# Optimization experiments

Hardware: AMD Instinct MI355X
Metric: run time of the kernel (lower is better)

The kernel has to match this reference:

```python
import jax, jax.numpy as jnp
import numpy as np
from jax import lax

DIM = 128
DEPTH = 2
OUT_DIM = 256
DIM_HEAD = 64
HEADS = 8
WS = 16
INNER = DIM_HEAD * HEADS
EPS = 1e-5
SCALE = DIM_HEAD ** (-0.5)


def setup_inputs() -> dict:
    key = jax.random.key(0)
    ks = jax.random.split(key, 20)
    s = 0.02
    L = DEPTH
    inp = {
        "x": jax.random.normal(ks[0], (1, DIM, 256, 256), dtype=jnp.float32),
        "ln1_g": jnp.ones((L, DIM), dtype=jnp.float32),
        "ln1_b": jnp.zeros((L, DIM), dtype=jnp.float32),
        "wq": jax.random.normal(ks[1], (L, INNER, DIM), dtype=jnp.float32) * s,
        "wkv": jax.random.normal(ks[2], (L, 2 * INNER, DIM), dtype=jnp.float32) * s,
        "wo": jax.random.normal(ks[3], (L, DIM, INNER), dtype=jnp.float32) * s,
        "bo": jnp.zeros((L, DIM), dtype=jnp.float32),
        "ln2_g": jnp.ones((L, DIM), dtype=jnp.float32),
        "ln2_b": jnp.zeros((L, DIM), dtype=jnp.float32),
        "w_in": jax.random.normal(ks[4], (L, DIM, DIM), dtype=jnp.float32) * s,
        "b_in": jnp.zeros((L, DIM), dtype=jnp.float32),
        "w_c3": jax.random.normal(ks[5], (L, OUT_DIM, DIM, 3, 3), dtype=jnp.float32) * s,
        "b_c3": jnp.zeros((L, OUT_DIM), dtype=jnp.float32),
        "w_c1": jax.random.normal(ks[6], (L, DIM, OUT_DIM), dtype=jnp.float32) * s,
        "b_c1": jnp.zeros((L, DIM), dtype=jnp.float32),
        "w_outer": jax.random.normal(ks[7], (DIM, DIM), dtype=jnp.float32) * s,
        "b_outer": jnp.zeros((DIM,), dtype=jnp.float32),
    }
    return inp


def _layernorm(x, g, b):
    # channel-wise (dim=1) norm; note torch code uses (std + eps), not sqrt(var + eps)
    mean = jnp.mean(x, axis=1, keepdims=True)
    std = jnp.sqrt(jnp.var(x, axis=1, keepdims=True))
    return (x - mean) / (std + EPS) * g[None, :, None, None] + b[None, :, None, None]


def _conv1x1(w, x, b=None):
    y = jnp.einsum('oi,bihw->bohw', w, x)
    if b is not None:
        y = y + b[None, :, None, None]
    return y


def _to_windows(t, B, H, W):
    # [B, HEADS*DIM_HEAD, H, W] -> [B*HEADS*nx*ny, WS*WS, DIM_HEAD]
    nx, ny = H // WS, W // WS
    t = t.reshape(B, HEADS, DIM_HEAD, nx, WS, ny, WS)
    t = t.transpose(0, 1, 3, 5, 4, 6, 2)
    return t.reshape(B * HEADS * nx * ny, WS * WS, DIM_HEAD)


def _from_windows(t, B, H, W):
    nx, ny = H // WS, W // WS
    t = t.reshape(B, HEADS, nx, ny, WS, WS, DIM_HEAD)
    t = t.transpose(0, 1, 6, 2, 4, 3, 5)
    return t.reshape(B, HEADS * DIM_HEAD, H, W)


def _attention(x, wq_l, wkv_l, wo_l, bo_l):
    B, _, H, W = x.shape
    q = _conv1x1(wq_l, x)
    kv = _conv1x1(wkv_l, x)
    k, v = kv[:, :INNER], kv[:, INNER:]
    q = _to_windows(q, B, H, W)
    k = _to_windows(k, B, H, W)
    v = _to_windows(v, B, H, W)
    sim = jnp.einsum('bid,bjd->bij', q, k) * SCALE  # [nwin, 256, 256]
    attn = jax.nn.softmax(sim, axis=-1)
    out = jnp.einsum('bij,bjd->bid', attn, v)
    out = _from_windows(out, B, H, W)
    return _conv1x1(wo_l, out, bo_l)


def _feedforward(x, w_in_l, b_in_l, w_c3_l, b_c3_l, w_c1_l, b_c1_l):
    h = _conv1x1(w_in_l, x, b_in_l)
    h = lax.conv_general_dilated(h, w_c3_l, window_strides=(1, 1), padding='SAME',
                                 dimension_numbers=('NCHW', 'OIHW', 'NCHW'))
    h = h + b_c3_l[None, :, None, None]
    h = jax.nn.gelu(h, approximate=False)
    return _conv1x1(w_c1_l, h, b_c1_l)


def reference(x, ln1_g, ln1_b, wq, wkv, wo, bo, ln2_g, ln2_b,
              w_in, b_in, w_c3, b_c3, w_c1, b_c1, w_outer, b_outer):
    for l in range(DEPTH):
        xn = _layernorm(x, ln1_g[l], ln1_b[l])
        x = _attention(xn, wq[l], wkv[l], wo[l], bo[l]) + x
        xn = _layernorm(x, ln2_g[l], ln2_b[l])
        x = _feedforward(xn, w_in[l], b_in[l], w_c3[l], b_c3[l], w_c1[l], b_c1[l]) + x
    return _conv1x1(w_outer, x, b_outer) + x
```

## Files before the change

### kernel.cpp

```cpp
#include <hip/hip_runtime.h>
#include <hip/hip_bf16.h>
#include <math.h>

typedef __hip_bfloat16 bf16;
typedef float f4 __attribute__((ext_vector_type(4)));
typedef short s8 __attribute__((ext_vector_type(8)));
typedef unsigned int u2 __attribute__((ext_vector_type(2)));
typedef unsigned int u4v __attribute__((ext_vector_type(4)));

__device__ __forceinline__ void gload16(const void* g, char* l) {
  __builtin_amdgcn_global_load_lds(
      (const __attribute__((address_space(1))) unsigned int*)g,
      (__attribute__((address_space(3))) unsigned int*)l, 16, 0, 0);
}
__device__ __forceinline__ unsigned short bfr(float f) {
  bf16 h = __float2bfloat16(f);
  return *(unsigned short*)&h;
}
__device__ __forceinline__ unsigned int pk2(float a, float b) {
  return (unsigned int)bfr(a) | ((unsigned int)bfr(b) << 16);
}
__device__ __forceinline__ unsigned int pkt(float a, float b) {
  return __builtin_amdgcn_perm(__float_as_uint(b), __float_as_uint(a), 0x07060302u);
}

__global__ __launch_bounds__(256) void prep_w(
    const float* __restrict__ wq, const float* __restrict__ wkv,
    const float* __restrict__ wo, const float* __restrict__ win,
    const float* __restrict__ wc3, const float* __restrict__ wc1,
    const float* __restrict__ wout, ushort* __restrict__ cw)
{
  int i = blockIdx.x * 256 + threadIdx.x;
  float v;
  if (i < 131072) v = wq[i];
  else if (i < 393216) v = wkv[i - 131072];
  else if (i < 524288) v = wo[i - 393216];
  else if (i < 557056) v = win[i - 524288];
  else if (i < 1146880) {
    int j = i - 557056; int lyr = j / 294912; int r = j - lyr * 294912;
    int m = r / 1152; int k = r - m * 1152; int tap = k >> 7; int ic = k & 127;
    v = wc3[(((size_t)lyr * 256 + m) * 128 + ic) * 9 + tap];
  }
  else if (i < 1212416) v = wc1[i - 1146880];
  else if (i < 1228800) v = wout[i - 1212416];
  else if (i < 1230848) { cw[i] = 0; return; }
  else return;
  cw[i] = bfr(v);
}

__global__ __launch_bounds__(256) void transpose_in(
    const float* __restrict__ x, float* __restrict__ xh)
{
  __shared__ float T[128][65];
  const int n0 = blockIdx.x * 64;
#pragma unroll
  for (int i = 0; i < 32; ++i) {
    int idx = i * 256 + threadIdx.x;
    int c = idx >> 6, nn = idx & 63;
    T[c][nn] = x[(size_t)c * 65536 + n0 + nn];
  }
  __syncthreads();
#pragma unroll
  for (int i = 0; i < 32; ++i) {
    int idx = i * 256 + threadIdx.x;
    int nn = idx >> 7, c = idx & 127;
    xh[(size_t)(n0 + nn) * 128 + c] = T[c][nn];
  }
}

__global__ __launch_bounds__(256) void ln_nhwc(
    const float* __restrict__ x, const float* __restrict__ g,
    const float* __restrict__ b, ushort* __restrict__ y)
{
  const int p = blockIdx.x * 256 + threadIdx.x;
  const f4* base = (const f4*)(x + (size_t)p * 128);
  f4 v[32];
  float s = 0.f, s2 = 0.f;
#pragma unroll
  for (int i = 0; i < 32; ++i) {
    v[i] = base[i];
#pragma unroll
    for (int j = 0; j < 4; ++j) { s += v[i][j]; s2 += v[i][j] * v[i][j]; }
  }
  float mean = s * (1.f / 128.f);
  float var = s2 * (1.f / 128.f) - mean * mean;
  var = var > 0.f ? var : 0.f;
  float inv = 1.f / (sqrtf(var) + 1e-5f);
  u2* dst = (u2*)(y + (size_t)p * 128);
#pragma unroll
  for (int i = 0; i < 32; ++i) {
    f4 gg = *(const f4*)(g + i * 4);
    f4 bb = *(const f4*)(b + i * 4);
    float f0 = (v[i][0] - mean) * inv * gg[0] + bb[0];
    float f1 = (v[i][1] - mean) * inv * gg[1] + bb[1];
    float f2 = (v[i][2] - mean) * inv * gg[2] + bb[2];
    float f3 = (v[i][3] - mean) * inv * gg[3] + bb[3];
    u2 st; st.x = pk2(f0, f1); st.y = pk2(f2, f3);
    dst[i] = st;
  }
}

__global__ __launch_bounds__(256) void to_bf16(
    const float* __restrict__ x, ushort* __restrict__ o)
{
  int i = blockIdx.x * 256 + threadIdx.x;
  f4 v = *(const f4*)(x + (size_t)i * 4);
  u2 st; st.x = pk2(v[0], v[1]); st.y = pk2(v[2], v[3]);
  *(u2*)(o + (size_t)i * 4) = st;
}

template<int MODE>
__global__ __launch_bounds__(256) void gemm_nhwc(
    const ushort* __restrict__ A, const ushort* __restrict__ X,
    const float* __restrict__ bias, const float* __restrict__ res,
    void* __restrict__ out, const int K, const int M)
{
  __shared__ __align__(16) char sm[32768];
  const int tid = threadIdx.x, w = tid >> 6, l = tid & 63;
  const int quad = l >> 4, l15 = l & 15;
  const int n0 = blockIdx.x * 128, m0 = blockIdx.y * 128;
  const int mh = (w & 1) * 64, nh = (w >> 1) * 64;
  const f4 fz = {0.f, 0.f, 0.f, 0.f};
  f4 acc[4][4];
#pragma unroll
  for (int a = 0; a < 4; ++a)
#pragma unroll
    for (int b2 = 0; b2 < 4; ++b2) acc[a][b2] = fz;

  const int KI = K >> 6;
  for (int kk = 0; kk < KI; ++kk) {
    if (kk) __syncthreads();
    const int k0 = kk << 6;
#pragma unroll
    for (int j = 0; j < 4; ++j) {
      int p = j * 256 + tid, r = p >> 3, c = (p & 7) ^ (r & 7);
      gload16(A + (size_t)(m0 + r) * K + k0 + c * 8, sm + (j * 256 + w * 64) * 16);
    }
#pragma unroll
    for (int j = 0; j < 4; ++j) {
      int p = j * 256 + tid, r = p >> 3, c = (p & 7) ^ (r & 7);
      gload16(X + (size_t)(n0 + r) * K + k0 + c * 8, sm + 16384 + (j * 256 + w * 64) * 16);
    }
    __syncthreads();
#pragma unroll
    for (int ks = 0; ks < 2; ++ks) {
      s8 af[4], bx[4];
#pragma unroll
      for (int mt = 0; mt < 4; ++mt) {
        int rr = mh + mt * 16 + l15;
        af[mt] = *(const s8*)(sm + rr * 128 + (((ks * 4 + quad) ^ (rr & 7)) << 4));
      }
#pragma unroll
      for (int nt = 0; nt < 4; ++nt) {
        int rr = nh + nt * 16 + l15;
        bx[nt] = *(const s8*)(sm + 16384 + rr * 128 + (((ks * 4 + quad) ^ (rr & 7)) << 4));
      }
#pragma unroll
      for (int mt = 0; mt < 4; ++mt)
#pragma unroll
        for (int nt = 0; nt < 4; ++nt)
          acc[mt][nt] = __builtin_amdgcn_mfma_f32_16x16x32_bf16(af[mt], bx[nt], acc[mt][nt], 0, 0, 0);
    }
  }
#pragma unroll
  for (int mt = 0; mt < 4; ++mt) {
#pragma unroll
    for (int nt = 0; nt < 4; ++nt) {
      const int m = m0 + mh + mt * 16 + quad * 4;
      const int n = n0 + nh + nt * 16 + l15;
      f4 bb = *(const f4*)(bias + m);
      f4 v = acc[mt][nt] + bb;
      if constexpr (MODE == 0) {
        u2 st; st.x = pk2(v[0], v[1]); st.y = pk2(v[2], v[3]);
        *(u2*)((ushort*)out + (size_t)n * M + m) = st;
      } else if constexpr (MODE == 1) {
        f4 r = *(const f4*)(res + (size_t)n * M + m);
        v += r;
        *(f4*)((float*)out + (size_t)n * M + m) = v;
      } else {
        f4 r = *(const f4*)(res + (size_t)n * M + m);
#pragma unroll
        for (int i = 0; i < 4; ++i)
          ((float*)out)[(size_t)(m + i) * 65536 + n] = v[i] + r[i];
      }
    }
  }
}

__global__ __launch_bounds__(256) void conv3_kernel(
    const ushort* __restrict__ A, const ushort* __restrict__ X,
    const float* __restrict__ bias, ushort* __restrict__ out,
    const ushort* __restrict__ zp)
{
  __shared__ __align__(16) char sm[32768];
  const int tid = threadIdx.x, w = tid >> 6, l = tid & 63;
  const int quad = l >> 4, l15 = l & 15;
  const int n0 = blockIdx.x * 128, m0 = blockIdx.y * 128;
  const int mh = (w & 1) * 64, nh = (w >> 1) * 64;
  const f4 fz = {0.f, 0.f, 0.f, 0.f};
  f4 acc[4][4];
#pragma unroll
  for (int a = 0; a < 4; ++a)
#pragma unroll
    for (int b2 = 0; b2 < 4; ++b2) acc[a][b2] = fz;

  for (int kk = 0; kk < 18; ++kk) {
    if (kk) __syncthreads();
    const int tap = kk >> 1, ky = tap / 3, kx = tap - ky * 3;
    const int dn = (ky - 1) * 256 + (kx - 1);
    const int kseg = (kk & 1) << 6;
#pragma unroll
    for (int j = 0; j < 4; ++j) {
      int p = j * 256 + tid, r = p >> 3, c = (p & 7) ^ (r & 7);
      gload16(A + (size_t)(m0 + r) * 1152 + kk * 64 + c * 8, sm + (j * 256 + w * 64) * 16);
    }
#pragma unroll
    for (int j = 0; j < 4; ++j) {
      int p = j * 256 + tid, r = p >> 3, c = (p & 7) ^ (r & 7);
      int nl = n0 + r;
      int ys = (nl >> 8) + ky - 1, xs = (nl & 255) + kx - 1;
      const ushort* gp = ((unsigned)ys < 256u && (unsigned)xs < 256u)
                         ? X + (size_t)(nl + dn) * 128 + kseg + c * 8 : zp;
      gload16(gp, sm + 16384 + (j * 256 + w * 64) * 16);
    }
    __syncthreads();
#pragma unroll
    for (int ks = 0; ks < 2; ++ks) {
      s8 af[4], bx[4];
#pragma unroll
      for (int mt = 0; mt < 4; ++mt) {
        int rr = mh + mt * 16 + l15;
        af[mt] = *(const s8*)(sm + rr * 128 + (((ks * 4 + quad) ^ (rr & 7)) << 4));
      }
#pragma unroll
      for (int nt = 0; nt < 4; ++nt) {
        int rr = nh + nt * 16 + l15;
        bx[nt] = *(const s8*)(sm + 16384 + rr * 128 + (((ks * 4 + quad) ^ (rr & 7)) << 4));
      }
#pragma unroll
      for (int mt = 0; mt < 4; ++mt)
#pragma unroll
        for (int nt = 0; nt < 4; ++nt)
          acc[mt][nt] = __builtin_amdgcn_mfma_f32_16x16x32_bf16(af[mt], bx[nt], acc[mt][nt], 0, 0, 0);
    }
  }
#pragma unroll
  for (int mt = 0; mt < 4; ++mt) {
#pragma unroll
    for (int nt = 0; nt < 4; ++nt) {
      const int m = m0 + mh + mt * 16 + quad * 4;
      const int n = n0 + nh + nt * 16 + l15;
      f4 bb = *(const f4*)(bias + m);
      f4 v = acc[mt][nt] + bb;
      float g0 = 0.5f * v[0] * (1.f + erff(v[0] * 0.70710678118f));
      float g1 = 0.5f * v[1] * (1.f + erff(v[1] * 0.70710678118f));
      float g2 = 0.5f * v[2] * (1.f + erff(v[2] * 0.70710678118f));
      float g3 = 0.5f * v[3] * (1.f + erff(v[3] * 0.70710678118f));
      u2 st; st.x = pk2(g0, g1); st.y = pk2(g2, g3);
      *(u2*)(out + (size_t)n * 256 + m) = st;
    }
  }
}

__global__ __launch_bounds__(512) void attn_kernel(
    const ushort* __restrict__ xn, const ushort* __restrict__ wq,
    const ushort* __restrict__ wkv, ushort* __restrict__ ao)
{
  __shared__ __align__(16) char sm[147456];
  const int tid = threadIdx.x, w = tid >> 6, l = tid & 63;
  const int quad = l >> 4, l15 = l & 15;
  const int win = blockIdx.x, head = blockIdx.y;
  const int nbase = ((win >> 4) << 12) + ((win & 15) << 4);
  char* RX = sm;
  char* RW = sm + 65536;
  char* RQ = sm + 81920;
  char* RK = sm + 114688;
  char* RVT = sm;
  char* Pw = sm + 32768 + w * 4096;
  const f4 fz = {0.f, 0.f, 0.f, 0.f};

#pragma unroll
  for (int j = 0; j < 8; ++j) {
    int p = j * 512 + tid, r = p >> 4, c = (p & 15) ^ (r & 15);
    int n = nbase + ((r >> 4) << 8) + (r & 15);
    gload16(xn + (size_t)n * 128 + c * 8, RX + (j * 512 + w * 64) * 16);
  }
  const ushort* wpq = wq + (size_t)head * 64 * 128;
#pragma unroll
  for (int j = 0; j < 2; ++j) {
    int p = j * 512 + tid, r = p >> 4, c = (p & 15) ^ (r & 15);
    gload16(wpq + (size_t)r * 128 + c * 8, RW + (j * 512 + w * 64) * 16);
  }
  __syncthreads();

  {
    f4 acc[4][2];
#pragma unroll
    for (int a = 0; a < 4; ++a) { acc[a][0] = fz; acc[a][1] = fz; }
#pragma unroll
    for (int ks = 0; ks < 4; ++ks) {
      s8 af[4], bx[2];
#pragma unroll
      for (int mt = 0; mt < 4; ++mt) {
        int rr = mt * 16 + l15;
        af[mt] = *(const s8*)(RW + rr * 256 + (((ks * 4 + quad) ^ (rr & 15)) << 4));
      }
#pragma unroll
      for (int nt = 0; nt < 2; ++nt) {
        int rr = w * 32 + nt * 16 + l15;
        bx[nt] = *(const s8*)(RX + rr * 256 + (((ks * 4 + quad) ^ (rr & 15)) << 4));
      }
#pragma unroll
      for (int mt = 0; mt < 4; ++mt)
#pragma unroll
        for (int nt = 0; nt < 2; ++nt)
          acc[mt][nt] = __builtin_amdgcn_mfma_f32_16x16x32_bf16(af[mt], bx[nt], acc[mt][nt], 0, 0, 0);
    }
#pragma unroll
    for (int mt = 0; mt < 4; ++mt)
#pragma unroll
      for (int nt = 0; nt < 2; ++nt) {
        int tok = w * 32 + nt * 16 + l15, d0 = mt * 16 + quad * 4;
        char* a = RQ + tok * 128 + (((d0 >> 3) ^ (tok & 7)) << 4) + (d0 & 7) * 2;
        *(unsigned int*)a = pkt(acc[mt][nt][0], acc[mt][nt][1]);
        *(unsigned int*)(a + 4) = pkt(acc[mt][nt][2], acc[mt][nt][3]);
      }
  }
  __syncthreads();
  const ushort* wpk = wkv + (size_t)head * 64 * 128;
#pragma unroll
  for (int j = 0; j < 2; ++j) {
    int p = j * 512 + tid, r = p >> 4, c = (p & 15) ^ (r & 15);
    gload16(wpk + (size_t)r * 128 + c * 8, RW + (j * 512 + w * 64) * 16);
  }
  __syncthreads();

  {
    f4 acc[4][2];
#pragma unroll
    for (int a = 0; a < 4; ++a) { acc[a][0] = fz; acc[a][1] = fz; }
#pragma unroll
    for (int ks = 0; ks < 4; ++ks) {
      s8 af[4], bx[2];
#pragma unroll
      for (int mt = 0; mt < 4; ++mt) {
        int rr = mt * 16 + l15;
        af[mt] = *(const s8*)(RW + rr * 256 + (((ks * 4 + quad) ^ (rr & 15)) << 4));
      }
#pragma unroll
      for (int nt = 0; nt < 2; ++nt) {
        int rr = w * 32 + nt * 16 + l15;
        bx[nt] = *(const s8*)(RX + rr * 256 + (((ks * 4 + quad) ^ (rr & 15)) << 4));
      }
#pragma unroll
      for (int mt = 0; mt < 4; ++mt)
#pragma unroll
        for (int nt = 0; nt < 2; ++nt)
          acc[mt][nt] = __builtin_amdgcn_mfma_f32_16x16x32_bf16(af[mt], bx[nt], acc[mt][nt], 0, 0, 0);
    }
#pragma unroll
    for (int mt = 0; mt < 4; ++mt)
#pragma unroll
      for (int nt = 0; nt < 2; ++nt) {
        int tok = w * 32 + nt * 16 + l15, d0 = mt * 16 + quad * 4;
        char* a = RK + tok * 128 + (((d0 >> 3) ^ (tok & 7)) << 4) + (d0 & 7) * 2;
        *(unsigned int*)a = pkt(acc[mt][nt][0], acc[mt][nt][1]);
        *(unsigned int*)(a + 4) = pkt(acc[mt][nt][2], acc[mt][nt][3]);
      }
  }
  __syncthreads();
  const ushort* wpv = wkv + (size_t)(512 + head * 64) * 128;
#pragma unroll
  for (int j = 0; j < 2; ++j) {
    int p = j * 512 + tid, r = p >> 4, c = (p & 15) ^ (r & 15);
    gload16(wpv + (size_t)r * 128 + c * 8, RW + (j * 512 + w * 64) * 16);
  }
  __syncthreads();

  {
    f4 acc[2][4];
#pragma unroll
    for (int a = 0; a < 2; ++a)
#pragma unroll
      for (int b2 = 0; b2 < 4; ++b2) acc[a][b2] = fz;
#pragma unroll
    for (int ks = 0; ks < 4; ++ks) {
      s8 ax[2], bw[4];
#pragma unroll
      for (int mt = 0; mt < 2; ++mt) {
        int rr = w * 32 + mt * 16 + l15;
        ax[mt] = *(const s8*)(RX + rr * 256 + (((ks * 4 + quad) ^ (rr & 15)) << 4));
      }
#pragma unroll
      for (int nt = 0; nt < 4; ++nt) {
        int rr = nt * 16 + l15;
        bw[nt] = *(const s8*)(RW + rr * 256 + (((ks * 4 + quad) ^ (rr & 15)) << 4));
      }
#pragma unroll
      for (int mt = 0; mt < 2; ++mt)
#pragma unroll
        for (int nt = 0; nt < 4; ++nt)
          acc[mt][nt] = __builtin_amdgcn_mfma_f32_16x16x32_bf16(ax[mt], bw[nt], acc[mt][nt], 0, 0, 0);
    }
    __syncthreads();
#pragma unroll
    for (int mt = 0; mt < 2; ++mt)
#pragma unroll
      for (int nt = 0; nt < 4; ++nt) {
        int d = nt * 16 + l15, t0 = w * 32 + mt * 16 + quad * 4;
        char* a = RVT + d * 512 + (((t0 >> 3) ^ (d & 31)) << 4) + (t0 & 7) * 2;
        *(unsigned int*)a = pkt(acc[mt][nt][0], acc[mt][nt][1]);
        *(unsigned int*)(a + 4) = pkt(acc[mt][nt][2], acc[mt][nt][3]);
      }
  }
  __syncthreads();

  f4 o[4][2];
  float lsum[2] = {0.f, 0.f};
#pragma unroll
  for (int a = 0; a < 4; ++a) { o[a][0] = fz; o[a][1] = fz; }

  for (int jt = 0; jt < 4; ++jt) {
    f4 s[4][2];
#pragma unroll
    for (int a = 0; a < 4; ++a) { s[a][0] = fz; s[a][1] = fz; }
#pragma unroll
    for (int ks = 0; ks < 2; ++ks) {
      s8 af[4], bq[2];
#pragma unroll
      for (int mt = 0; mt < 4; ++mt) {
        int rr = jt * 64 + mt * 16 + l15;
        af[mt] = *(const s8*)(RK + rr * 128 + (((ks * 4 + quad) ^ (rr & 7)) << 4));
      }
#pragma unroll
      for (int nt = 0; nt < 2; ++nt) {
        int rr = w * 32 + nt * 16 + l15;
        bq[nt] = *(const s8*)(RQ + rr * 128 + (((ks * 4 + quad) ^ (rr & 7)) << 4));
      }
#pragma unroll
      for (int mt = 0; mt < 4; ++mt)
#pragma unroll
        for (int nt = 0; nt < 2; ++nt)
          s[mt][nt] = __builtin_amdgcn_mfma_f32_16x16x32_bf16(af[mt], bq[nt], s[mt][nt], 0, 0, 0);
    }
#pragma unroll
    for (int mt = 0; mt < 4; ++mt)
#pragma unroll
      for (int nt = 0; nt < 2; ++nt) {
        float p0 = exp2f(s[mt][nt][0] * 0.18033688f);
        float p1 = exp2f(s[mt][nt][1] * 0.18033688f);
        float p2 = exp2f(s[mt][nt][2] * 0.18033688f);
        float p3 = exp2f(s[mt][nt][3] * 0.18033688f);
        lsum[nt] += p0 + p1 + p2 + p3;
        int iL = nt * 16 + l15, j0 = mt * 16 + quad * 4;
        char* a = Pw + iL * 128 + (((j0 >> 3) ^ (iL & 7)) << 4) + (j0 & 7) * 2;
        *(unsigned int*)a = pkt(p0, p1);
        *(unsigned int*)(a + 4) = pkt(p2, p3);
      }
#pragma unroll
    for (int ks = 0; ks < 2; ++ks) {
      s8 av[4], bp[2];
#pragma unroll
      for (int mt = 0; mt < 4; ++mt) {
        int d = mt * 16 + l15;
        av[mt] = *(const s8*)(RVT + d * 512 + (((jt * 8 + ks * 4 + quad) ^ (d & 31)) << 4));
      }
#pragma unroll
      for (int nt = 0; nt < 2; ++nt) {
        int iL = nt * 16 + l15;
        bp[nt] = *(const s8*)(Pw + iL * 128 + (((ks * 4 + quad) ^ (iL & 7)) << 4));
      }
#pragma unroll
      for (int mt = 0; mt < 4; ++mt)
#pragma unroll
        for (int nt = 0; nt < 2; ++nt)
          o[mt][nt] = __builtin_amdgcn_mfma_f32_16x16x32_bf16(av[mt], bp[nt], o[mt][nt], 0, 0, 0);
    }
  }

  float inv[2];
#pragma unroll
  for (int nt = 0; nt < 2; ++nt) {
    float v = lsum[nt];
    v += __shfl_xor(v, 16, 64);
    v += __shfl_xor(v, 32, 64);
    inv[nt] = 1.f / v;
  }
  __syncthreads();
#pragma unroll
  for (int mt = 0; mt < 4; ++mt)
#pragma unroll
    for (int nt = 0; nt < 2; ++nt) {
      int i = w * 32 + nt * 16 + l15, d0 = mt * 16 + quad * 4;
      char* a = RQ + i * 128 + (((d0 >> 3) ^ (i & 7)) << 4) + (d0 & 7) * 2;
      *(unsigned int*)a = pkt(o[mt][nt][0] * inv[nt], o[mt][nt][1] * inv[nt]);
      *(unsigned int*)(a + 4) = pkt(o[mt][nt][2] * inv[nt], o[mt][nt][3] * inv[nt]);
    }
  __syncthreads();
  const int tok = tid >> 1, half = tid & 1;
  const int n = nbase + ((tok >> 4) << 8) + (tok & 15);
  ushort* dst = ao + (size_t)n * 512 + head * 64 + half * 32;
#pragma unroll
  for (int c = 0; c < 4; ++c) {
    u4v v = *(const u4v*)(RQ + tok * 128 + (((half * 4 + c) ^ (tok & 7)) << 4));
    *(u4v*)(dst + c * 8) = v;
  }
}

extern "C" void kernel_launch(void* const* d_in, const int* in_sizes, int n_in,
                              void* d_out, int out_size, void* d_ws, size_t ws_size,
                              hipStream_t stream)
{
  const float* x_in    = (const float*)d_in[0];
  const float* ln1_g   = (const float*)d_in[1];
  const float* ln1_b   = (const float*)d_in[2];
  const float* wq      = (const float*)d_in[3];
  const float* wkv     = (const float*)d_in[4];
  const float* wo      = (const float*)d_in[5];
  const float* bo      = (const float*)d_in[6];
  const float* ln2_g   = (const float*)d_in[7];
  const float* ln2_b   = (const float*)d_in[8];
  const float* w_in    = (const float*)d_in[9];
  const float* b_in    = (const float*)d_in[10];
  const float* w_c3    = (const float*)d_in[11];
  const float* b_c3    = (const float*)d_in[12];
  const float* w_c1    = (const float*)d_in[13];
  const float* b_c1    = (const float*)d_in[14];
  const float* w_outer = (const float*)d_in[15];
  const float* b_outer = (const float*)d_in[16];

  char* wsb = (char*)d_ws;
  ushort* CW = (ushort*)wsb;
  float*  XH = (float*)(wsb + 4194304);
  ushort* XN = (ushort*)(wsb + 37748736);
  ushort* AO = (ushort*)(wsb + 54525952);
  ushort* H  = (ushort*)(wsb + 121634816);
  ushort* G  = (ushort*)(wsb + 138412032);
  ushort* XB = (ushort*)(wsb + 171966464);

  const ushort* zp = CW + 1228800;
  dim3 b256(256);

  prep_w<<<dim3(4808), b256, 0, stream>>>(wq, wkv, wo, w_in, w_c3, w_c1, w_outer, CW);
  transpose_in<<<dim3(1024), b256, 0, stream>>>(x_in, XH);

  for (int lyr = 0; lyr < 2; ++lyr) {
    const ushort* cwq = CW + lyr * 65536;
    const ushort* cwkv = CW + 131072 + lyr * 131072;
    const ushort* cwo = CW + 393216 + lyr * 65536;
    const ushort* cwin = CW + 524288 + lyr * 16384;
    const ushort* cw3 = CW + 557056 + lyr * 294912;
    const ushort* cwc1 = CW + 1146880 + lyr * 32768;

    ln_nhwc<<<dim3(256), b256, 0, stream>>>(XH, ln1_g + lyr * 128, ln1_b + lyr * 128, XN);
    attn_kernel<<<dim3(256, 8), dim3(512), 0, stream>>>(XN, cwq, cwkv, AO);
    gemm_nhwc<1><<<dim3(512, 1), b256, 0, stream>>>(cwo, AO, bo + lyr * 128, XH, XH, 512, 128);
    ln_nhwc<<<dim3(256), b256, 0, stream>>>(XH, ln2_g + lyr * 128, ln2_b + lyr * 128, XN);
    gemm_nhwc<0><<<dim3(512, 1), b256, 0, stream>>>(cwin, XN, b_in + lyr * 128, nullptr, H, 128, 128);
    conv3_kernel<<<dim3(512, 2), b256, 0, stream>>>(cw3, H, b_c3 + lyr * 256, G, zp);
    gemm_nhwc<1><<<dim3(512, 1), b256, 0, stream>>>(cwc1, G, b_c1 + lyr * 128, XH, XH, 256, 128);
  }
  to_bf16<<<dim3(8192), b256, 0, stream>>>(XH, XB);
  gemm_nhwc<2><<<dim3(512, 1), b256, 0, stream>>>(CW + 1212416, XB, b_outer, XH, d_out, 128, 128);
}
```

Before: 666.5 us.

## Fuse input transpose and bf16 cast into neighbors; preload all attention weights

Removes the standalone NCHW→NHWC transpose by having the first layernorm read NCHW directly and the first output-projection GEMM read the NCHW residual. Removes the to_bf16 pass by having the last FFN GEMM also emit a bf16 copy. In the attention kernel, Q/K/V weights are loaded up front into separate LDS regions, and Q fragments are kept in registers via lane shuffles rather than staged through LDS, which drops several barriers and reload phases. The strided NCHW reads in layernorm and the residual epilogue are less coalesced, and keeping Q in registers raises register pressure in the attention kernel.

```diff
diff --git a/kernel.cpp b/kernel.cpp
--- a/kernel.cpp
+++ b/kernel.cpp
@@ -48,39 +48,30 @@
   cw[i] = bfr(v);
 }
 
-__global__ __launch_bounds__(256) void transpose_in(
-    const float* __restrict__ x, float* __restrict__ xh)
-{
-  __shared__ float T[128][65];
-  const int n0 = blockIdx.x * 64;
-#pragma unroll
-  for (int i = 0; i < 32; ++i) {
-    int idx = i * 256 + threadIdx.x;
-    int c = idx >> 6, nn = idx & 63;
-    T[c][nn] = x[(size_t)c * 65536 + n0 + nn];
-  }
-  __syncthreads();
-#pragma unroll
-  for (int i = 0; i < 32; ++i) {
-    int idx = i * 256 + threadIdx.x;
-    int nn = idx >> 7, c = idx & 127;
-    xh[(size_t)(n0 + nn) * 128 + c] = T[c][nn];
-  }
-}
-
+template<bool NCHW>
 __global__ __launch_bounds__(256) void ln_nhwc(
     const float* __restrict__ x, const float* __restrict__ g,
     const float* __restrict__ b, ushort* __restrict__ y)
 {
   const int p = blockIdx.x * 256 + threadIdx.x;
-  const f4* base = (const f4*)(x + (size_t)p * 128);
   f4 v[32];
   float s = 0.f, s2 = 0.f;
-#pragma unroll
-  for (int i = 0; i < 32; ++i) {
-    v[i] = base[i];
-#pragma unroll
-    for (int j = 0; j < 4; ++j) { s += v[i][j]; s2 += v[i][j] * v[i][j]; }
+  if constexpr (NCHW) {
+#pragma unroll
+    for (int i = 0; i < 32; ++i)
+#pragma unroll
+      for (int j = 0; j < 4; ++j) {
+        float t = x[(size_t)(i * 4 + j) * 65536 + p];
+        v[i][j] = t; s += t; s2 += t * t;
+      }
+  } else {
+    const f4* base = (const f4*)(x + (size_t)p * 128);
+#pragma unroll
+    for (int i = 0; i < 32; ++i) {
+      v[i] = base[i];
+#pragma unroll
+      for (int j = 0; j < 4; ++j) { s += v[i][j]; s2 += v[i][j] * v[i][j]; }
+    }
   }
   float mean = s * (1.f / 128.f);
   float var = s2 * (1.f / 128.f) - mean * mean;
@@ -100,20 +91,11 @@
   }
 }
 
-__global__ __launch_bounds__(256) void to_bf16(
-    const float* __restrict__ x, ushort* __restrict__ o)
-{
-  int i = blockIdx.x * 256 + threadIdx.x;
-  f4 v = *(const f4*)(x + (size_t)i * 4);
-  u2 st; st.x = pk2(v[0], v[1]); st.y = pk2(v[2], v[3]);
-  *(u2*)(o + (size_t)i * 4) = st;
-}
-
 template<int MODE>
 __global__ __launch_bounds__(256) void gemm_nhwc(
     const ushort* __restrict__ A, const ushort* __restrict__ X,
     const float* __restrict__ bias, const float* __restrict__ res,
-    void* __restrict__ out, const int K, const int M)
+    void* __restrict__ out, ushort* __restrict__ out2, const int K, const int M)
 {
   __shared__ __align__(16) char sm[32768];
   const int tid = threadIdx.x, w = tid >> 6, l = tid & 63;
@@ -173,8 +155,18 @@
       if constexpr (MODE == 0) {
         u2 st; st.x = pk2(v[0], v[1]); st.y = pk2(v[2], v[3]);
         *(u2*)((ushort*)out + (size_t)n * M + m) = st;
-      } else if constexpr (MODE == 1) {
+      } else if constexpr (MODE == 1 || MODE == 3) {
         f4 r = *(const f4*)(res + (size_t)n * M + m);
+        v += r;
+        *(f4*)((float*)out + (size_t)n * M + m) = v;
+        if constexpr (MODE == 3) {
+          u2 st; st.x = pk2(v[0], v[1]); st.y = pk2(v[2], v[3]);
+          *(u2*)(out2 + (size_t)n * M + m) = st;
+        }
+      } else if constexpr (MODE == 4) {
+        f4 r;
+#pragma unroll
+        for (int i = 0; i < 4; ++i) r[i] = res[(size_t)(m + i) * 65536 + n];
         v += r;
         *(f4*)((float*)out + (size_t)n * M + m) = v;
       } else {
@@ -271,12 +263,12 @@
   const int quad = l >> 4, l15 = l & 15;
   const int win = blockIdx.x, head = blockIdx.y;
   const int nbase = ((win >> 4) << 12) + ((win & 15) << 4);
-  char* RX = sm;
-  char* RW = sm + 65536;
-  char* RQ = sm + 81920;
-  char* RK = sm + 114688;
+  char* RX  = sm;
+  char* RW  = sm + 65536;
+  char* RK  = sm + 114688;
   char* RVT = sm;
-  char* Pw = sm + 32768 + w * 4096;
+  char* Pw  = sm + 32768 + w * 4096;
+  char* RO  = RW;
   const f4 fz = {0.f, 0.f, 0.f, 0.f};
 
 #pragma unroll
@@ -285,14 +277,29 @@
     int n = nbase + ((r >> 4) << 8) + (r & 15);
     gload16(xn + (size_t)n * 128 + c * 8, RX + (j * 512 + w * 64) * 16);
   }
-  const ushort* wpq = wq + (size_t)head * 64 * 128;
-#pragma unroll
-  for (int j = 0; j < 2; ++j) {
-    int p = j * 512 + tid, r = p >> 4, c = (p & 15) ^ (r & 15);
-    gload16(wpq + (size_t)r * 128 + c * 8, RW + (j * 512 + w * 64) * 16);
+  {
+    const ushort* wpq = wq + (size_t)head * 64 * 128;
+    const ushort* wpk = wkv + (size_t)head * 64 * 128;
+    const ushort* wpv = wkv + (size_t)(512 + head * 64) * 128;
+#pragma unroll
+    for (int j = 0; j < 2; ++j) {
+      int p = j * 512 + tid, r = p >> 4, c = (p & 15) ^ (r & 15);
+      gload16(wpq + (size_t)r * 128 + c * 8, RW + (j * 512 + w * 64) * 16);
+    }
+#pragma unroll
+    for (int j = 0; j < 2; ++j) {
+      int p = j * 512 + tid, r = p >> 4, c = (p & 15) ^ (r & 15);
+      gload16(wpk + (size_t)r * 128 + c * 8, RW + 16384 + (j * 512 + w * 64) * 16);
+    }
+#pragma unroll
+    for (int j = 0; j < 2; ++j) {
+      int p = j * 512 + tid, r = p >> 4, c = (p & 15) ^ (r & 15);
+      gload16(wpv + (size_t)r * 128 + c * 8, RW + 32768 + (j * 512 + w * 64) * 16);
+    }
   }
   __syncthreads();
 
+  s8 bq[2][2];
   {
     f4 acc[4][2];
 #pragma unroll
@@ -317,23 +324,27 @@
           acc[mt][nt] = __builtin_amdgcn_mfma_f32_16x16x32_bf16(af[mt], bx[nt], acc[mt][nt], 0, 0, 0);
     }
 #pragma unroll
-    for (int mt = 0; mt < 4; ++mt)
-#pragma unroll
-      for (int nt = 0; nt < 2; ++nt) {
-        int tok = w * 32 + nt * 16 + l15, d0 = mt * 16 + quad * 4;
-        char* a = RQ + tok * 128 + (((d0 >> 3) ^ (tok & 7)) << 4) + (d0 & 7) * 2;
-        *(unsigned int*)a = pkt(acc[mt][nt][0], acc[mt][nt][1]);
-        *(unsigned int*)(a + 4) = pkt(acc[mt][nt][2], acc[mt][nt][3]);
-      }
-  }
-  __syncthreads();
-  const ushort* wpk = wkv + (size_t)head * 64 * 128;
-#pragma unroll
-  for (int j = 0; j < 2; ++j) {
-    int p = j * 512 + tid, r = p >> 4, c = (p & 15) ^ (r & 15);
-    gload16(wpk + (size_t)r * 128 + c * 8, RW + (j * 512 + w * 64) * 16);
-  }
-  __syncthreads();
+    for (int nt = 0; nt < 2; ++nt) {
+      unsigned pd[4][2];
+#pragma unroll
+      for (int mt = 0; mt < 4; ++mt) {
+        pd[mt][0] = pkt(acc[mt][nt][0], acc[mt][nt][1]);
+        pd[mt][1] = pkt(acc[mt][nt][2], acc[mt][nt][3]);
+      }
+#pragma unroll
+      for (int ks = 0; ks < 2; ++ks) {
+        u4v t;
+#pragma unroll
+        for (int dj = 0; dj < 4; ++dj) {
+          int srcl = l15 + (((quad & 1) * 2 + (dj >> 1)) << 4);
+          unsigned va = (unsigned)__shfl((int)pd[2 * ks][dj & 1], srcl, 64);
+          unsigned vb = (unsigned)__shfl((int)pd[2 * ks + 1][dj & 1], srcl, 64);
+          t[dj] = (quad < 2) ? va : vb;
+        }
+        bq[nt][ks] = __builtin_bit_cast(s8, t);
+      }
+    }
+  }
 
   {
     f4 acc[4][2];
@@ -345,7 +356,7 @@
 #pragma unroll
       for (int mt = 0; mt < 4; ++mt) {
         int rr = mt * 16 + l15;
-        af[mt] = *(const s8*)(RW + rr * 256 + (((ks * 4 + quad) ^ (rr & 15)) << 4));
+        af[mt] = *(const s8*)(RW + 16384 + rr * 256 + (((ks * 4 + quad) ^ (rr & 15)) << 4));
       }
 #pragma unroll
       for (int nt = 0; nt < 2; ++nt) {
@@ -368,14 +379,6 @@
         *(unsigned int*)(a + 4) = pkt(acc[mt][nt][2], acc[mt][nt][3]);
       }
   }
-  __syncthreads();
-  const ushort* wpv = wkv + (size_t)(512 + head * 64) * 128;
-#pragma unroll
-  for (int j = 0; j < 2; ++j) {
-    int p = j * 512 + tid, r = p >> 4, c = (p & 15) ^ (r & 15);
-    gload16(wpv + (size_t)r * 128 + c * 8, RW + (j * 512 + w * 64) * 16);
-  }
-  __syncthreads();
 
   {
     f4 acc[2][4];
@@ -394,7 +397,7 @@
 #pragma unroll
       for (int nt = 0; nt < 4; ++nt) {
         int rr = nt * 16 + l15;
-        bw[nt] = *(const s8*)(RW + rr * 256 + (((ks * 4 + quad) ^ (rr & 15)) << 4));
+        bw[nt] = *(const s8*)(RW + 32768 + rr * 256 + (((ks * 4 + quad) ^ (rr & 15)) << 4));
       }
 #pragma unroll
       for (int mt = 0; mt < 2; ++mt)
@@ -426,22 +429,17 @@
     for (int a = 0; a < 4; ++a) { s[a][0] = fz; s[a][1] = fz; }
 #pragma unroll
     for (int ks = 0; ks < 2; ++ks) {
-      s8 af[4], bq[2];
+      s8 af[4];
 #pragma unroll
       for (int mt = 0; mt < 4; ++mt) {
         int rr = jt * 64 + mt * 16 + l15;
         af[mt] = *(const s8*)(RK + rr * 128 + (((ks * 4 + quad) ^ (rr & 7)) << 4));
       }
 #pragma unroll
-      for (int nt = 0; nt < 2; ++nt) {
-        int rr = w * 32 + nt * 16 + l15;
-        bq[nt] = *(const s8*)(RQ + rr * 128 + (((ks * 4 + quad) ^ (rr & 7)) << 4));
-      }
-#pragma unroll
       for (int mt = 0; mt < 4; ++mt)
 #pragma unroll
         for (int nt = 0; nt < 2; ++nt)
-          s[mt][nt] = __builtin_amdgcn_mfma_f32_16x16x32_bf16(af[mt], bq[nt], s[mt][nt], 0, 0, 0);
+          s[mt][nt] = __builtin_amdgcn_mfma_f32_16x16x32_bf16(af[mt], bq[nt][ks], s[mt][nt], 0, 0, 0);
     }
 #pragma unroll
     for (int mt = 0; mt < 4; ++mt)
@@ -486,13 +484,12 @@
     v += __shfl_xor(v, 32, 64);
     inv[nt] = 1.f / v;
   }
-  __syncthreads();
 #pragma unroll
   for (int mt = 0; mt < 4; ++mt)
 #pragma unroll
     for (int nt = 0; nt < 2; ++nt) {
       int i = w * 32 + nt * 16 + l15, d0 = mt * 16 + quad * 4;
-      char* a = RQ + i * 128 + (((d0 >> 3) ^ (i & 7)) << 4) + (d0 & 7) * 2;
+      char* a = RO + i * 128 + (((d0 >> 3) ^ (i & 7)) << 4) + (d0 & 7) * 2;
       *(unsigned int*)a = pkt(o[mt][nt][0] * inv[nt], o[mt][nt][1] * inv[nt]);
       *(unsigned int*)(a + 4) = pkt(o[mt][nt][2] * inv[nt], o[mt][nt][3] * inv[nt]);
     }
@@ -502,7 +499,7 @@
   ushort* dst = ao + (size_t)n * 512 + head * 64 + half * 32;
 #pragma unroll
   for (int c = 0; c < 4; ++c) {
-    u4v v = *(const u4v*)(RQ + tok * 128 + (((half * 4 + c) ^ (tok & 7)) << 4));
+    u4v v = *(const u4v*)(RO + tok * 128 + (((half * 4 + c) ^ (tok & 7)) << 4));
     *(u4v*)(dst + c * 8) = v;
   }
 }
@@ -542,7 +539,6 @@
   dim3 b256(256);
 
   prep_w<<<dim3(4808), b256, 0, stream>>>(wq, wkv, wo, w_in, w_c3, w_c1, w_outer, CW);
-  transpose_in<<<dim3(1024), b256, 0, stream>>>(x_in, XH);
 
   for (int lyr = 0; lyr < 2; ++lyr) {
     const ushort* cwq = CW + lyr * 65536;
@@ -552,14 +548,26 @@
     const ushort* cw3 = CW + 557056 + lyr * 294912;
     const ushort* cwc1 = CW + 1146880 + lyr * 32768;
 
-    ln_nhwc<<<dim3(256), b256, 0, stream>>>(XH, ln1_g + lyr * 128, ln1_b + lyr * 128, XN);
+    if (lyr == 0)
+      ln_nhwc<true><<<dim3(256), b256, 0, stream>>>(x_in, ln1_g, ln1_b, XN);
+    else
+      ln_nhwc<false><<<dim3(256), b256, 0, stream>>>(XH, ln1_g + lyr * 128, ln1_b + lyr * 128, XN);
+
     attn_kernel<<<dim3(256, 8), dim3(512), 0, stream>>>(XN, cwq, cwkv, AO);
-    gemm_nhwc<1><<<dim3(512, 1), b256, 0, stream>>>(cwo, AO, bo + lyr * 128, XH, XH, 512, 128);
-    ln_nhwc<<<dim3(256), b256, 0, stream>>>(XH, ln2_g + lyr * 128, ln2_b + lyr * 128, XN);
-    gemm_nhwc<0><<<dim3(512, 1), b256, 0, stream>>>(cwin, XN, b_in + lyr * 128, nullptr, H, 128, 128);
+
+    if (lyr == 0)
+      gemm_nhwc<4><<<dim3(512, 1), b256, 0, stream>>>(cwo, AO, bo, x_in, XH, nullptr, 512, 128);
+    else
+      gemm_nhwc<1><<<dim3(512, 1), b256, 0, stream>>>(cwo, AO, bo + lyr * 128, XH, XH, nullptr, 512, 128);
+
+    ln_nhwc<false><<<dim3(256), b256, 0, stream>>>(XH, ln2_g + lyr * 128, ln2_b + lyr * 128, XN);
+    gemm_nhwc<0><<<dim3(512, 1), b256, 0, stream>>>(cwin, XN, b_in + lyr * 128, nullptr, H, nullptr, 128, 128);
     conv3_kernel<<<dim3(512, 2), b256, 0, stream>>>(cw3, H, b_c3 + lyr * 256, G, zp);
-    gemm_nhwc<1><<<dim3(512, 1), b256, 0, stream>>>(cwc1, G, b_c1 + lyr * 128, XH, XH, 256, 128);
-  }
-  to_bf16<<<dim3(8192), b256, 0, stream>>>(XH, XB);
-  gemm_nhwc<2><<<dim3(512, 1), b256, 0, stream>>>(CW + 1212416, XB, b_outer, XH, d_out, 128, 128);
-}
+
+    if (lyr == 1)
+      gemm_nhwc<3><<<dim3(512, 1), b256, 0, stream>>>(cwc1, G, b_c1 + lyr * 128, XH, XH, XB, 256, 128);
+    else
+      gemm_nhwc<1><<<dim3(512, 1), b256, 0, stream>>>(cwc1, G, b_c1 + lyr * 128, XH, XH, nullptr, 256, 128);
+  }
+  gemm_nhwc<2><<<dim3(512, 1), b256, 0, stream>>>(CW + 1212416, XB, b_outer, XH, d_out, nullptr, 128, 128);
+}
```

After: 649.7 us. 2.5% less time.
